# Kernel tuning notes

Measured on AMD Instinct MI355X. Metric: run time of the kernel, lower is better.

## Reference

```python
import jax, jax.numpy as jnp
import numpy as np

B, S, H, V = 64, 512, 1024, 50257


def setup_inputs() -> dict:
    key = jax.random.key(0)
    ks = jax.random.split(key, 12)
    s = 0.02
    return {
        "input_ids": jax.random.randint(ks[0], (B,), 0, V),
        "hidden": jax.random.normal(ks[1], (1, B, H), jnp.float32),
        "encoder_outputs": jax.random.normal(ks[2], (B, S, H), jnp.float32),
        "emb": jax.random.normal(ks[3], (V, H), jnp.float32) * s,
        "attn_w": jax.random.normal(ks[4], (H, 2 * H), jnp.float32) * s,
        "attn_b": jnp.zeros((H,), jnp.float32),
        "v_w": jax.random.normal(ks[5], (H,), jnp.float32) * s,
        "w_ih": jax.random.normal(ks[6], (3 * H, 2 * H), jnp.float32) * s,
        "w_hh": jax.random.normal(ks[7], (3 * H, H), jnp.float32) * s,
        "b_ih": jnp.zeros((3 * H,), jnp.float32),
        "b_hh": jnp.zeros((3 * H,), jnp.float32),
        "out_w": jax.random.normal(ks[8], (V, H), jnp.float32) * s,
        "out_b": jnp.zeros((V,), jnp.float32),
    }


def reference(input_ids, hidden, encoder_outputs, emb, attn_w, attn_b, v_w,
              w_ih, w_hh, b_ih, b_hh, out_w, out_b):
    # dropout disabled (eval mode)
    embedded = emb[input_ids]                       # [B,H]
    h = hidden[0]                                   # [B,H] (single-layer GRU)

    # Bahdanau attention: score = v^T tanh(W [h; enc])
    h_rep = jnp.broadcast_to(h[:, None, :], encoder_outputs.shape)  # [B,S,H]
    cat = jnp.concatenate([h_rep, encoder_outputs], axis=2)         # [B,S,2H]
    energy = jnp.tanh(jnp.einsum('bsk,hk->bsh', cat, attn_w) + attn_b)
    scores = jnp.einsum('bsh,h->bs', energy, v_w)
    attn = jax.nn.softmax(scores, axis=1)                            # [B,S]
    context = jnp.einsum('bs,bsh->bh', attn, encoder_outputs)        # [B,H]

    # one GRU step (PyTorch gate order: r, z, n)
    x = jnp.concatenate([embedded, context], axis=1)                 # [B,2H]
    gi = x @ w_ih.T + b_ih                                           # [B,3H]
    gh = h @ w_hh.T + b_hh                                           # [B,3H]
    i_r, i_z, i_n = jnp.split(gi, 3, axis=1)
    h_r, h_z, h_n = jnp.split(gh, 3, axis=1)
    r = jax.nn.sigmoid(i_r + h_r)
    z = jax.nn.sigmoid(i_z + h_z)
    n = jnp.tanh(i_n + r * h_n)
    h_new = (1.0 - z) * n + z * h                                    # [B,H]

    prediction = h_new @ out_w.T + out_b                             # [B,V]
    return prediction, h_new[None], attn
```

## Files before the change

### kernel.cpp

```cpp
#include <hip/hip_runtime.h>
#include <math.h>

#define H_ 1024
#define S_ 512
#define B_ 64
#define V_ 50257

typedef unsigned short u16;
typedef __bf16 bf16x8 __attribute__((ext_vector_type(8)));
typedef u16 us8 __attribute__((ext_vector_type(8)));
typedef float f32x4 __attribute__((ext_vector_type(4)));

__device__ __forceinline__ u16 f2bf(float f) {
  union { float f; unsigned u; } v; v.f = f;
  unsigned u = v.u;
  u += 0x7fffu + ((u >> 16) & 1u);
  return (u16)(u >> 16);
}
__device__ __forceinline__ float bf2f(u16 s) {
  union { unsigned u; float f; } v; v.u = ((unsigned)s) << 16;
  return v.f;
}
__device__ __forceinline__ void gld16(const void* g, void* l) {
  __builtin_amdgcn_global_load_lds(
      (__attribute__((address_space(1))) void*)g,
      (__attribute__((address_space(3))) void*)l, 16, 0, 0);
}

__global__ __launch_bounds__(256) void prep_enc(const float* __restrict__ enc,
                                                u16* __restrict__ encbf) {
  size_t i = ((size_t)blockIdx.x * 256 + threadIdx.x) * 8;
  float4 f0 = *(const float4*)(enc + i);
  float4 f1 = *(const float4*)(enc + i + 4);
  us8 u = { f2bf(f0.x), f2bf(f0.y), f2bf(f0.z), f2bf(f0.w),
            f2bf(f1.x), f2bf(f1.y), f2bf(f1.z), f2bf(f1.w) };
  *(us8*)(encbf + i) = u;
}

__global__ __launch_bounds__(256) void prep_w2(const float* __restrict__ attnw,
                                               u16* __restrict__ w2bf) {
  size_t i = ((size_t)blockIdx.x * 256 + threadIdx.x) * 8;
  int n = (int)(i >> 10), k = (int)(i & 1023);
  const float* src = attnw + (size_t)n * 2048 + 1024 + k;
  float4 f0 = *(const float4*)(src);
  float4 f1 = *(const float4*)(src + 4);
  us8 u = { f2bf(f0.x), f2bf(f0.y), f2bf(f0.z), f2bf(f0.w),
            f2bf(f1.x), f2bf(f1.y), f2bf(f1.z), f2bf(f1.w) };
  *(us8*)(w2bf + i) = u;
}

__global__ __launch_bounds__(256) void zero_all(float* __restrict__ s) {
  size_t i = ((size_t)blockIdx.x * 256 + threadIdx.x) * 4;
  *(float4*)(s + i) = make_float4(0.f, 0.f, 0.f, 0.f);
}

__global__ __launch_bounds__(256) void prep_xh(const int* __restrict__ ids,
                                               const float* __restrict__ emb,
                                               const float* __restrict__ hidden,
                                               u16* __restrict__ xh) {
  int b = blockIdx.x, t = threadIdx.x;
  int idx = t * 4;
  const float* er = emb + (size_t)ids[b] * H_;
  const float* hr = hidden + (size_t)b * H_;
  float4 e = *(const float4*)(er + idx);
  float4 h = *(const float4*)(hr + idx);
  ushort4 ue = { f2bf(e.x), f2bf(e.y), f2bf(e.z), f2bf(e.w) };
  ushort4 uh = { f2bf(h.x), f2bf(h.y), f2bf(h.z), f2bf(h.w) };
  *(ushort4*)(xh + (size_t)b * 3072 + idx) = ue;
  *(ushort4*)(xh + (size_t)b * 3072 + 2048 + idx) = uh;
}

__global__ __launch_bounds__(256) void mfma_m64(const u16* __restrict__ A, int lda,
                                                const float* __restrict__ B, int ldb,
                                                int kchunk, const float* __restrict__ bias,
                                                float* __restrict__ out, int ldout) {
  __shared__ __align__(16) u16 As[64 * 32];
  __shared__ __align__(16) u16 Bs[128 * 32];
  const int t = threadIdx.x;
  const int n0 = blockIdx.x * 128;
  const int kbase = blockIdx.y * kchunk;
  const int lane = t & 63, wid = t >> 6;
  const int col = lane & 15, quad = lane >> 4;
  f32x4 acc[4][2] = {};

  const int arow = t >> 2, acol = (t & 3) * 8;
  const int brow = t >> 1, bcol = (t & 1) * 16;
  const float* gB = B + (size_t)(n0 + brow) * ldb + kbase + bcol;
  const u16* gA = A + (size_t)arow * lda + kbase + acol;

  for (int k0 = 0; k0 < kchunk; k0 += 32) {
    gld16(gA + k0, &As[t * 8]);
    float4 f0 = *(const float4*)(gB + k0);
    float4 f1 = *(const float4*)(gB + k0 + 4);
    float4 f2 = *(const float4*)(gB + k0 + 8);
    float4 f3 = *(const float4*)(gB + k0 + 12);
    us8 u0 = { f2bf(f0.x), f2bf(f0.y), f2bf(f0.z), f2bf(f0.w),
               f2bf(f1.x), f2bf(f1.y), f2bf(f1.z), f2bf(f1.w) };
    us8 u1 = { f2bf(f2.x), f2bf(f2.y), f2bf(f2.z), f2bf(f2.w),
               f2bf(f3.x), f2bf(f3.y), f2bf(f3.z), f2bf(f3.w) };
    *(us8*)&Bs[brow * 32 + bcol] = u0;
    *(us8*)&Bs[brow * 32 + bcol + 8] = u1;
    __syncthreads();
    bf16x8 af[4], bfr[2];
#pragma unroll
    for (int i = 0; i < 4; i++)
      af[i] = *(const bf16x8*)&As[(i * 16 + col) * 32 + quad * 8];
#pragma unroll
    for (int j = 0; j < 2; j++)
      bfr[j] = *(const bf16x8*)&Bs[(wid * 32 + j * 16 + col) * 32 + quad * 8];
#pragma unroll
    for (int i = 0; i < 4; i++)
#pragma unroll
      for (int j = 0; j < 2; j++)
        acc[i][j] = __builtin_amdgcn_mfma_f32_16x16x32_bf16(af[i], bfr[j], acc[i][j], 0, 0, 0);
    __syncthreads();
  }
#pragma unroll
  for (int j = 0; j < 2; j++) {
    int n = n0 + wid * 32 + j * 16 + col;
    float bb = (bias != nullptr && blockIdx.y == 0) ? bias[n] : 0.f;
#pragma unroll
    for (int i = 0; i < 4; i++)
#pragma unroll
      for (int r = 0; r < 4; r++) {
        int m = i * 16 + quad * 4 + r;
        atomicAdd(&out[(size_t)m * ldout + n], acc[i][j][r] + bb);
      }
  }
}

__global__ __launch_bounds__(256) void attn_gemm(const u16* __restrict__ encbf,
                                                 const u16* __restrict__ w2bf,
                                                 const float* __restrict__ hW1,
                                                 const float* __restrict__ vw,
                                                 float* __restrict__ scores) {
  __shared__ __align__(16) u16 As[128 * 32];
  __shared__ __align__(16) u16 Bs[128 * 32];
  const int t = threadIdx.x;
  const int n0 = blockIdx.x * 128;
  const int m0 = blockIdx.y * 128;
  const int lane = t & 63, wid = t >> 6;
  const int wm = (wid >> 1) * 64, wn = (wid & 1) * 64;
  const int col = lane & 15, quad = lane >> 4;

  f32x4 acc[4][4] = {};

  const int srow = t >> 2, scol8 = (t & 3) * 8;
  const u16* ga = encbf + (size_t)(m0 + srow) * H_ + scol8;
  const u16* gb = w2bf + (size_t)(n0 + srow) * H_ + scol8;
  u16* la = &As[t * 8];
  u16* lb = &Bs[t * 8];

  for (int k0 = 0; k0 < H_; k0 += 32) {
    gld16(ga + k0, la);
    gld16(ga + k0 + (size_t)64 * H_, la + 2048);
    gld16(gb + k0, lb);
    gld16(gb + k0 + (size_t)64 * H_, lb + 2048);
    __syncthreads();
    bf16x8 af[4], bfr[4];
#pragma unroll
    for (int i = 0; i < 4; i++)
      af[i] = *(const bf16x8*)&As[(wm + i * 16 + col) * 32 + quad * 8];
#pragma unroll
    for (int j = 0; j < 4; j++)
      bfr[j] = *(const bf16x8*)&Bs[(wn + j * 16 + col) * 32 + quad * 8];
#pragma unroll
    for (int i = 0; i < 4; i++)
#pragma unroll
      for (int j = 0; j < 4; j++)
        acc[i][j] = __builtin_amdgcn_mfma_f32_16x16x32_bf16(af[i], bfr[j], acc[i][j], 0, 0, 0);
    __syncthreads();
  }

  const int b = m0 >> 9;
  float sp[4][4] = {{0.f}};
#pragma unroll
  for (int j = 0; j < 4; j++) {
    int n = n0 + wn + j * 16 + col;
    float hw = hW1[(size_t)b * H_ + n];
    float w = vw[n];
#pragma unroll
    for (int i = 0; i < 4; i++)
#pragma unroll
      for (int r = 0; r < 4; r++)
        sp[i][r] += w * tanhf(acc[i][j][r] + hw);
  }
#pragma unroll
  for (int i = 0; i < 4; i++)
#pragma unroll
    for (int r = 0; r < 4; r++) {
      float v = sp[i][r];
      v += __shfl_xor(v, 1, 64);
      v += __shfl_xor(v, 2, 64);
      v += __shfl_xor(v, 4, 64);
      v += __shfl_xor(v, 8, 64);
      if (col == 0) {
        int m = m0 + wm + i * 16 + quad * 4 + r;
        atomicAdd(&scores[m], v);
      }
    }
}

__global__ __launch_bounds__(256) void softmax_ctx(const float* __restrict__ scores,
                                                   const u16* __restrict__ encbf,
                                                   float* __restrict__ attn_out,
                                                   u16* __restrict__ xh) {
  __shared__ float sc[512];
  __shared__ float redm[4], reds[4];
  int b = blockIdx.x, t = threadIdx.x;
  int lane = t & 63, wid = t >> 6;
  float s0 = scores[b * 512 + t];
  float s1 = scores[b * 512 + 256 + t];
  float mx = fmaxf(s0, s1);
  for (int off = 32; off; off >>= 1) mx = fmaxf(mx, __shfl_xor(mx, off, 64));
  if (lane == 0) redm[wid] = mx;
  __syncthreads();
  float bm = fmaxf(fmaxf(redm[0], redm[1]), fmaxf(redm[2], redm[3]));
  float e0 = expf(s0 - bm), e1 = expf(s1 - bm);
  float sm = e0 + e1;
  for (int off = 32; off; off >>= 1) sm += __shfl_xor(sm, off, 64);
  if (lane == 0) reds[wid] = sm;
  __syncthreads();
  float inv = 1.f / (reds[0] + reds[1] + reds[2] + reds[3]);
  float a0v = e0 * inv, a1v = e1 * inv;
  sc[t] = a0v; sc[t + 256] = a1v;
  attn_out[b * 512 + t] = a0v;
  attn_out[b * 512 + 256 + t] = a1v;
  __syncthreads();

  int h0 = t * 4;
  const u16* ep = encbf + (size_t)b * S_ * H_ + h0;
  float p0 = 0.f, p1 = 0.f, p2 = 0.f, p3 = 0.f;
  float q0 = 0.f, q1 = 0.f, q2 = 0.f, q3 = 0.f;
  for (int s = 0; s < S_; s += 2) {
    ushort4 ua = *(const ushort4*)(ep + (size_t)s * H_);
    ushort4 ub = *(const ushort4*)(ep + (size_t)(s + 1) * H_);
    float wa = sc[s], wb = sc[s + 1];
    p0 += wa * bf2f(ua.x); p1 += wa * bf2f(ua.y); p2 += wa * bf2f(ua.z); p3 += wa * bf2f(ua.w);
    q0 += wb * bf2f(ub.x); q1 += wb * bf2f(ub.y); q2 += wb * bf2f(ub.z); q3 += wb * bf2f(ub.w);
  }
  ushort4 c = { f2bf(p0 + q0), f2bf(p1 + q1), f2bf(p2 + q2), f2bf(p3 + q3) };
  *(ushort4*)(xh + (size_t)b * 3072 + 1024 + h0) = c;
}

__global__ __launch_bounds__(256) void gru_gates(const float* __restrict__ gi,
                                                 const float* __restrict__ gh,
                                                 const float* __restrict__ bih,
                                                 const float* __restrict__ bhh,
                                                 const float* __restrict__ hprev,
                                                 float* __restrict__ hnew_out,
                                                 u16* __restrict__ hnew_bf) {
  int idx = blockIdx.x * 256 + threadIdx.x;
  int b = idx >> 10, h = idx & 1023;
  size_t base = (size_t)b * 3072 + h;
  float ir = gi[base] + bih[h];
  float iz = gi[base + 1024] + bih[H_ + h];
  float in_ = gi[base + 2048] + bih[2 * H_ + h];
  float hr = gh[base] + bhh[h];
  float hz = gh[base + 1024] + bhh[H_ + h];
  float hn = gh[base + 2048] + bhh[2 * H_ + h];
  float rg = 1.f / (1.f + expf(-(ir + hr)));
  float zg = 1.f / (1.f + expf(-(iz + hz)));
  float ng = tanhf(in_ + rg * hn);
  float hp = hprev[(size_t)b * H_ + h];
  float out = (1.f - zg) * ng + zg * hp;
  hnew_out[(size_t)b * H_ + h] = out;
  hnew_bf[(size_t)b * H_ + h] = f2bf(out);
}

__global__ __launch_bounds__(256) void pred_gemm(const u16* __restrict__ hnbf,
                                                 const float* __restrict__ outw,
                                                 const float* __restrict__ outb,
                                                 float* __restrict__ pred) {
  __shared__ __align__(16) u16 As[64 * 32];
  __shared__ __align__(16) u16 Bs[128 * 32];
  const int t = threadIdx.x;
  const int n0 = blockIdx.x * 128;
  const int lane = t & 63, wid = t >> 6;
  const int col = lane & 15, quad = lane >> 4;
  f32x4 acc[4][2] = {};

  const int arow = t >> 2, acol = (t & 3) * 8;
  const int brow = t >> 1, bcol = (t & 1) * 16;
  int gbrow = n0 + brow;
  if (gbrow >= V_) gbrow = V_ - 1;
  const float* gB = outw + (size_t)gbrow * H_ + bcol;
  const u16* gA = hnbf + (size_t)arow * H_ + acol;

  for (int k0 = 0; k0 < H_; k0 += 32) {
    gld16(gA + k0, &As[t * 8]);
    float4 f0 = *(const float4*)(gB + k0);
    float4 f1 = *(const float4*)(gB + k0 + 4);
    float4 f2 = *(const float4*)(gB + k0 + 8);
    float4 f3 = *(const float4*)(gB + k0 + 12);
    us8 u0 = { f2bf(f0.x), f2bf(f0.y), f2bf(f0.z), f2bf(f0.w),
               f2bf(f1.x), f2bf(f1.y), f2bf(f1.z), f2bf(f1.w) };
    us8 u1 = { f2bf(f2.x), f2bf(f2.y), f2bf(f2.z), f2bf(f2.w),
               f2bf(f3.x), f2bf(f3.y), f2bf(f3.z), f2bf(f3.w) };
    *(us8*)&Bs[brow * 32 + bcol] = u0;
    *(us8*)&Bs[brow * 32 + bcol + 8] = u1;
    __syncthreads();
    bf16x8 af[4], bfr[2];
#pragma unroll
    for (int i = 0; i < 4; i++)
      af[i] = *(const bf16x8*)&As[(i * 16 + col) * 32 + quad * 8];
#pragma unroll
    for (int j = 0; j < 2; j++)
      bfr[j] = *(const bf16x8*)&Bs[(wid * 32 + j * 16 + col) * 32 + quad * 8];
#pragma unroll
    for (int i = 0; i < 4; i++)
#pragma unroll
      for (int j = 0; j < 2; j++)
        acc[i][j] = __builtin_amdgcn_mfma_f32_16x16x32_bf16(af[i], bfr[j], acc[i][j], 0, 0, 0);
    __syncthreads();
  }
#pragma unroll
  for (int j = 0; j < 2; j++) {
    int vg = n0 + wid * 32 + j * 16 + col;
    if (vg < V_) {
      float bb = outb[vg];
#pragma unroll
      for (int i = 0; i < 4; i++)
#pragma unroll
        for (int r = 0; r < 4; r++) {
          int m = i * 16 + quad * 4 + r;
          pred[(size_t)m * V_ + vg] = acc[i][j][r] + bb;
        }
    }
  }
}

extern "C" void kernel_launch(void* const* d_in, const int* in_sizes, int n_in,
                              void* d_out, int out_size, void* d_ws, size_t ws_size,
                              hipStream_t stream) {
  const int* input_ids = (const int*)d_in[0];
  const float* hidden = (const float*)d_in[1];
  const float* enc = (const float*)d_in[2];
  const float* emb = (const float*)d_in[3];
  const float* attn_w = (const float*)d_in[4];
  const float* attn_b = (const float*)d_in[5];
  const float* v_w = (const float*)d_in[6];
  const float* w_ih = (const float*)d_in[7];
  const float* w_hh = (const float*)d_in[8];
  const float* b_ih = (const float*)d_in[9];
  const float* b_hh = (const float*)d_in[10];
  const float* out_w = (const float*)d_in[11];
  const float* out_b = (const float*)d_in[12];

  float* pred = (float*)d_out;
  float* hnew_out = pred + (size_t)B_ * V_;
  float* attn_out = hnew_out + (size_t)B_ * H_;

  char* ws = (char*)d_ws;
  u16* encbf = (u16*)ws;
  u16* w2bf = (u16*)(ws + 67108864);
  float* scores = (float*)(ws + 69206016);
  float* hW1 = (float*)(ws + 69337088);
  float* gi = (float*)(ws + 69599232);
  float* gh = (float*)(ws + 70385664);
  u16* xh = (u16*)(ws + 71172096);
  u16* hnbf = (u16*)(ws + 71565312);

  prep_enc<<<16384, 256, 0, stream>>>(enc, encbf);
  prep_w2<<<512, 256, 0, stream>>>(attn_w, w2bf);
  zero_all<<<480, 256, 0, stream>>>(scores);
  prep_xh<<<64, 256, 0, stream>>>(input_ids, emb, hidden, xh);
  mfma_m64<<<dim3(8, 4), 256, 0, stream>>>(xh + 2048, 3072, attn_w, 2048, 256,
                                           attn_b, hW1, 1024);
  attn_gemm<<<dim3(8, 256), 256, 0, stream>>>(encbf, w2bf, hW1, v_w, scores);
  softmax_ctx<<<64, 256, 0, stream>>>(scores, encbf, attn_out, xh);
  mfma_m64<<<dim3(24, 4), 256, 0, stream>>>(xh, 3072, w_ih, 2048, 512,
                                            nullptr, gi, 3072);
  mfma_m64<<<dim3(24, 4), 256, 0, stream>>>(xh + 2048, 3072, w_hh, 1024, 256,
                                            nullptr, gh, 3072);
  gru_gates<<<256, 256, 0, stream>>>(gi, gh, b_ih, b_hh, hidden, hnew_out, hnbf);
  pred_gemm<<<((V_ + 127) / 128), 256, 0, stream>>>(hnbf, out_w, out_b, pred);
}
```

Baseline: 705.1 us.

## Widen attention GEMM tile, swizzle LDS, fast tanh, split context and pred GEMM

The attention-score GEMM now uses 128x256 tiles with an XOR-swizzled LDS layout to cut bank conflicts, and replaces tanhf with an exp2/rcp approximation. The softmax-context kernel splits the hidden dimension across 4 blocks per batch and reduces sequence segments in shared memory, giving more parallelism. The output projection is split-K over two blocks that combine with atomics, which needs an extra kernel to zero the prediction buffer first. These changes add register pressure, atomic traffic and zeroing work, and the fast tanh is slightly less accurate.

After: 668.2 us. 5.2% less time.

```diff
diff --git a/kernel.cpp b/kernel.cpp
--- a/kernel.cpp
+++ b/kernel.cpp
@@ -25,6 +25,10 @@
   __builtin_amdgcn_global_load_lds(
       (__attribute__((address_space(1))) void*)g,
       (__attribute__((address_space(3))) void*)l, 16, 0, 0);
+}
+__device__ __forceinline__ float ftanh(float x) {
+  float e = __builtin_amdgcn_exp2f(x * 2.8853900817779268f);
+  return 1.f - 2.f * __builtin_amdgcn_rcpf(e + 1.f);
 }
 
 __global__ __launch_bounds__(256) void prep_enc(const float* __restrict__ enc,
@@ -52,6 +56,11 @@
 __global__ __launch_bounds__(256) void zero_all(float* __restrict__ s) {
   size_t i = ((size_t)blockIdx.x * 256 + threadIdx.x) * 4;
   *(float4*)(s + i) = make_float4(0.f, 0.f, 0.f, 0.f);
+}
+
+__global__ __launch_bounds__(256) void zero_pred(float* __restrict__ p, int n4) {
+  int i = blockIdx.x * 256 + threadIdx.x;
+  if (i < n4) *(float4*)(p + (size_t)i * 4) = make_float4(0.f, 0.f, 0.f, 0.f);
 }
 
 __global__ __launch_bounds__(256) void prep_xh(const int* __restrict__ ids,
@@ -129,45 +138,50 @@
   }
 }
 
-__global__ __launch_bounds__(256) void attn_gemm(const u16* __restrict__ encbf,
-                                                 const u16* __restrict__ w2bf,
-                                                 const float* __restrict__ hW1,
-                                                 const float* __restrict__ vw,
-                                                 float* __restrict__ scores) {
+__global__ __launch_bounds__(256, 2) void attn_gemm(const u16* __restrict__ encbf,
+                                                    const u16* __restrict__ w2bf,
+                                                    const float* __restrict__ hW1,
+                                                    const float* __restrict__ vw,
+                                                    float* __restrict__ scores) {
   __shared__ __align__(16) u16 As[128 * 32];
-  __shared__ __align__(16) u16 Bs[128 * 32];
+  __shared__ __align__(16) u16 Bs[256 * 32];
   const int t = threadIdx.x;
-  const int n0 = blockIdx.x * 128;
+  const int n0 = blockIdx.x * 256;
   const int m0 = blockIdx.y * 128;
   const int lane = t & 63, wid = t >> 6;
-  const int wm = (wid >> 1) * 64, wn = (wid & 1) * 64;
+  const int wm = (wid >> 1) * 64, wn = (wid & 1) * 128;
   const int col = lane & 15, quad = lane >> 4;
 
-  f32x4 acc[4][4] = {};
-
-  const int srow = t >> 2, scol8 = (t & 3) * 8;
-  const u16* ga = encbf + (size_t)(m0 + srow) * H_ + scol8;
-  const u16* gb = w2bf + (size_t)(n0 + srow) * H_ + scol8;
+  f32x4 acc[4][8] = {};
+
+  const int srow = t >> 2, kb = t & 3;
+  const int kbs = kb ^ ((srow >> 1) & 3);
+  const u16* ga = encbf + (size_t)(m0 + srow) * H_ + kbs * 8;
+  const u16* gb = w2bf + (size_t)(n0 + srow) * H_ + kbs * 8;
   u16* la = &As[t * 8];
   u16* lb = &Bs[t * 8];
+
+  const int q2 = quad ^ ((col >> 1) & 3);
 
   for (int k0 = 0; k0 < H_; k0 += 32) {
     gld16(ga + k0, la);
     gld16(ga + k0 + (size_t)64 * H_, la + 2048);
     gld16(gb + k0, lb);
     gld16(gb + k0 + (size_t)64 * H_, lb + 2048);
-    __syncthreads();
-    bf16x8 af[4], bfr[4];
-#pragma unroll
-    for (int i = 0; i < 4; i++)
-      af[i] = *(const bf16x8*)&As[(wm + i * 16 + col) * 32 + quad * 8];
-#pragma unroll
-    for (int j = 0; j < 4; j++)
-      bfr[j] = *(const bf16x8*)&Bs[(wn + j * 16 + col) * 32 + quad * 8];
-#pragma unroll
-    for (int i = 0; i < 4; i++)
-#pragma unroll
-      for (int j = 0; j < 4; j++)
+    gld16(gb + k0 + (size_t)128 * H_, lb + 4096);
+    gld16(gb + k0 + (size_t)192 * H_, lb + 6144);
+    __syncthreads();
+    bf16x8 af[4], bfr[8];
+#pragma unroll
+    for (int i = 0; i < 4; i++)
+      af[i] = *(const bf16x8*)&As[(wm + i * 16 + col) * 32 + q2 * 8];
+#pragma unroll
+    for (int j = 0; j < 8; j++)
+      bfr[j] = *(const bf16x8*)&Bs[(wn + j * 16 + col) * 32 + q2 * 8];
+#pragma unroll
+    for (int i = 0; i < 4; i++)
+#pragma unroll
+      for (int j = 0; j < 8; j++)
         acc[i][j] = __builtin_amdgcn_mfma_f32_16x16x32_bf16(af[i], bfr[j], acc[i][j], 0, 0, 0);
     __syncthreads();
   }
@@ -175,7 +189,7 @@
   const int b = m0 >> 9;
   float sp[4][4] = {{0.f}};
 #pragma unroll
-  for (int j = 0; j < 4; j++) {
+  for (int j = 0; j < 8; j++) {
     int n = n0 + wn + j * 16 + col;
     float hw = hW1[(size_t)b * H_ + n];
     float w = vw[n];
@@ -183,7 +197,7 @@
     for (int i = 0; i < 4; i++)
 #pragma unroll
       for (int r = 0; r < 4; r++)
-        sp[i][r] += w * tanhf(acc[i][j][r] + hw);
+        sp[i][r] += w * ftanh(acc[i][j][r] + hw);
   }
 #pragma unroll
   for (int i = 0; i < 4; i++)
@@ -207,7 +221,8 @@
                                                    u16* __restrict__ xh) {
   __shared__ float sc[512];
   __shared__ float redm[4], reds[4];
-  int b = blockIdx.x, t = threadIdx.x;
+  __shared__ __align__(16) float red[4][256];
+  int b = blockIdx.x, q = blockIdx.y, t = threadIdx.x;
   int lane = t & 63, wid = t >> 6;
   float s0 = scores[b * 512 + t];
   float s1 = scores[b * 512 + 256 + t];
@@ -224,23 +239,29 @@
   float inv = 1.f / (reds[0] + reds[1] + reds[2] + reds[3]);
   float a0v = e0 * inv, a1v = e1 * inv;
   sc[t] = a0v; sc[t + 256] = a1v;
-  attn_out[b * 512 + t] = a0v;
-  attn_out[b * 512 + 256 + t] = a1v;
+  if (q == 0) {
+    attn_out[b * 512 + t] = a0v;
+    attn_out[b * 512 + 256 + t] = a1v;
+  }
   __syncthreads();
 
-  int h0 = t * 4;
+  int sseg = t >> 6, hlane = t & 63;
+  int h0 = q * 256 + hlane * 4;
   const u16* ep = encbf + (size_t)b * S_ * H_ + h0;
+  int sbase = sseg * 128;
   float p0 = 0.f, p1 = 0.f, p2 = 0.f, p3 = 0.f;
-  float q0 = 0.f, q1 = 0.f, q2 = 0.f, q3 = 0.f;
-  for (int s = 0; s < S_; s += 2) {
-    ushort4 ua = *(const ushort4*)(ep + (size_t)s * H_);
-    ushort4 ub = *(const ushort4*)(ep + (size_t)(s + 1) * H_);
-    float wa = sc[s], wb = sc[s + 1];
+  float r0 = 0.f, r1 = 0.f, r2 = 0.f, r3 = 0.f;
+  for (int s = 0; s < 128; s += 2) {
+    ushort4 ua = *(const ushort4*)(ep + (size_t)(sbase + s) * H_);
+    ushort4 ub = *(const ushort4*)(ep + (size_t)(sbase + s + 1) * H_);
+    float wa = sc[sbase + s], wb = sc[sbase + s + 1];
     p0 += wa * bf2f(ua.x); p1 += wa * bf2f(ua.y); p2 += wa * bf2f(ua.z); p3 += wa * bf2f(ua.w);
-    q0 += wb * bf2f(ub.x); q1 += wb * bf2f(ub.y); q2 += wb * bf2f(ub.z); q3 += wb * bf2f(ub.w);
-  }
-  ushort4 c = { f2bf(p0 + q0), f2bf(p1 + q1), f2bf(p2 + q2), f2bf(p3 + q3) };
-  *(ushort4*)(xh + (size_t)b * 3072 + 1024 + h0) = c;
+    r0 += wb * bf2f(ub.x); r1 += wb * bf2f(ub.y); r2 += wb * bf2f(ub.z); r3 += wb * bf2f(ub.w);
+  }
+  *(float4*)&red[sseg][hlane * 4] = make_float4(p0 + r0, p1 + r1, p2 + r2, p3 + r3);
+  __syncthreads();
+  float sum = red[0][t] + red[1][t] + red[2][t] + red[3][t];
+  xh[(size_t)b * 3072 + 1024 + q * 256 + t] = f2bf(sum);
 }
 
 __global__ __launch_bounds__(256) void gru_gates(const float* __restrict__ gi,
@@ -276,6 +297,7 @@
   __shared__ __align__(16) u16 Bs[128 * 32];
   const int t = threadIdx.x;
   const int n0 = blockIdx.x * 128;
+  const int kbase = blockIdx.y * 512;
   const int lane = t & 63, wid = t >> 6;
   const int col = lane & 15, quad = lane >> 4;
   f32x4 acc[4][2] = {};
@@ -284,10 +306,10 @@
   const int brow = t >> 1, bcol = (t & 1) * 16;
   int gbrow = n0 + brow;
   if (gbrow >= V_) gbrow = V_ - 1;
-  const float* gB = outw + (size_t)gbrow * H_ + bcol;
-  const u16* gA = hnbf + (size_t)arow * H_ + acol;
-
-  for (int k0 = 0; k0 < H_; k0 += 32) {
+  const float* gB = outw + (size_t)gbrow * H_ + kbase + bcol;
+  const u16* gA = hnbf + (size_t)arow * H_ + kbase + acol;
+
+  for (int k0 = 0; k0 < 512; k0 += 32) {
     gld16(gA + k0, &As[t * 8]);
     float4 f0 = *(const float4*)(gB + k0);
     float4 f1 = *(const float4*)(gB + k0 + 4);
@@ -318,13 +340,13 @@
   for (int j = 0; j < 2; j++) {
     int vg = n0 + wid * 32 + j * 16 + col;
     if (vg < V_) {
-      float bb = outb[vg];
+      float bb = (blockIdx.y == 0) ? outb[vg] : 0.f;
 #pragma unroll
       for (int i = 0; i < 4; i++)
 #pragma unroll
         for (int r = 0; r < 4; r++) {
           int m = i * 16 + quad * 4 + r;
-          pred[(size_t)m * V_ + vg] = acc[i][j][r] + bb;
+          atomicAdd(&pred[(size_t)m * V_ + vg], acc[i][j][r] + bb);
         }
     }
   }
@@ -364,15 +386,16 @@
   prep_enc<<<16384, 256, 0, stream>>>(enc, encbf);
   prep_w2<<<512, 256, 0, stream>>>(attn_w, w2bf);
   zero_all<<<480, 256, 0, stream>>>(scores);
+  zero_pred<<<3142, 256, 0, stream>>>(pred, (B_ * V_) / 4);
   prep_xh<<<64, 256, 0, stream>>>(input_ids, emb, hidden, xh);
   mfma_m64<<<dim3(8, 4), 256, 0, stream>>>(xh + 2048, 3072, attn_w, 2048, 256,
                                            attn_b, hW1, 1024);
-  attn_gemm<<<dim3(8, 256), 256, 0, stream>>>(encbf, w2bf, hW1, v_w, scores);
-  softmax_ctx<<<64, 256, 0, stream>>>(scores, encbf, attn_out, xh);
+  attn_gemm<<<dim3(4, 256), 256, 0, stream>>>(encbf, w2bf, hW1, v_w, scores);
+  softmax_ctx<<<dim3(64, 4), 256, 0, stream>>>(scores, encbf, attn_out, xh);
   mfma_m64<<<dim3(24, 4), 256, 0, stream>>>(xh, 3072, w_ih, 2048, 512,
                                             nullptr, gi, 3072);
   mfma_m64<<<dim3(24, 4), 256, 0, stream>>>(xh + 2048, 3072, w_hh, 1024, 256,
                                             nullptr, gh, 3072);
   gru_gates<<<256, 256, 0, stream>>>(gi, gh, b_ih, b_hh, hidden, hnew_out, hnbf);
-  pred_gemm<<<((V_ + 127) / 128), 256, 0, stream>>>(hnbf, out_w, out_b, pred);
-}
+  pred_gemm<<<dim3((V_ + 127) / 128, 2), 256, 0, stream>>>(hnbf, out_w, out_b, pred);
+}
```
